# Optimization experiments

Measured on AMD Instinct MI355X. Metric: run time of the kernel, lower is better.

## Reference

```python
import jax, jax.numpy as jnp
import numpy as np

N_COMPANIES = 2000
HIDDEN = 256
HEADS = 8
LAYERS = 3
IN_DIM = 64
NEG_SLOPE = 0.2  # PyG GATConv default leaky_relu slope


def setup_inputs() -> dict:
    key = jax.random.key(0)
    ks = jax.random.split(key, 32)
    B, E = 64, 64000
    C = HIDDEN // HEADS
    emb_dim = HIDDEN // 4
    def lin(k, fo, fi):
        k1, k2 = jax.random.split(k)
        s = 1.0 / np.sqrt(fi)
        return (jax.random.uniform(k1, (fo, fi), jnp.float32, -s, s),
                jax.random.uniform(k2, (fo,), jnp.float32, -s, s))
    inp = {}
    inp['x'] = jax.random.normal(ks[0], (B, IN_DIM), jnp.float32)
    inp['company_indices'] = jax.random.randint(ks[1], (B,), 0, N_COMPANIES)
    inp['edge_index'] = jax.random.randint(ks[2], (2, E), 0, N_COMPANIES)
    inp['edge_attr'] = jax.random.uniform(ks[3], (E,), jnp.float32)
    inp['W_in'], inp['b_in'] = lin(ks[4], HIDDEN, IN_DIM)
    # stacked GAT params (all layers same shape)
    g = 0.05
    inp['gat_W'] = g * jax.random.normal(ks[5], (LAYERS, HEADS * C, HIDDEN), jnp.float32)
    inp['gat_att_src'] = g * jax.random.normal(ks[6], (LAYERS, HEADS, C), jnp.float32)
    inp['gat_att_dst'] = g * jax.random.normal(ks[7], (LAYERS, HEADS, C), jnp.float32)
    inp['gat_We'] = g * jax.random.normal(ks[8], (LAYERS, HEADS * C, 1), jnp.float32)
    inp['gat_att_edge'] = g * jax.random.normal(ks[9], (LAYERS, HEADS, C), jnp.float32)
    inp['gat_b'] = jnp.zeros((LAYERS, HEADS * C), jnp.float32)
    inp['emb'] = jax.random.normal(ks[10], (N_COMPANIES, emb_dim), jnp.float32)
    inp['W_fuse'], inp['b_fuse'] = lin(ks[11], HIDDEN, HIDDEN + emb_dim)
    inp['W_p1'], inp['b_p1'] = lin(ks[12], HIDDEN // 2, HIDDEN)
    inp['W_p2'], inp['b_p2'] = lin(ks[13], HIDDEN // 4, HIDDEN // 2)
    inp['W_p3'], inp['b_p3'] = lin(ks[14], 1, HIDDEN // 4)
    inp['W_d1'], inp['b_d1'] = lin(ks[15], HIDDEN // 2, HIDDEN)
    inp['W_d2'], inp['b_d2'] = lin(ks[16], HIDDEN // 4, HIDDEN // 2)
    inp['W_d3'], inp['b_d3'] = lin(ks[17], 1, HIDDEN // 4)
    return inp


def _gat_layer(xg, src, dst, ea, W, att_s, att_d, We, att_e, b, N):
    # xg: [N, F] node features; src/dst: [E2] (with self-loops); ea: [E2]
    H, C = att_s.shape
    xp = (xg @ W.T).reshape(N, H, C)
    a_s = jnp.sum(xp * att_s, -1)                       # [N, H]
    a_d = jnp.sum(xp * att_d, -1)                       # [N, H]
    ef = (ea[:, None] @ We.T).reshape(-1, H, C)         # [E2, H, C]
    a_e = jnp.sum(ef * att_e, -1)                       # [E2, H]
    logits = jax.nn.leaky_relu(a_s[src] + a_d[dst] + a_e, NEG_SLOPE)
    m = jax.ops.segment_max(logits, dst, num_segments=N)
    ex = jnp.exp(logits - m[dst])
    denom = jax.ops.segment_sum(ex, dst, num_segments=N)
    alpha = ex / (denom[dst] + 1e-16)                   # per-dst softmax
    out = jax.ops.segment_sum(alpha[:, :, None] * xp[src], dst, num_segments=N)
    return out.reshape(N, H * C) + b


def reference(x, company_indices, edge_index, edge_attr, W_in, b_in,
              gat_W, gat_att_src, gat_att_dst, gat_We, gat_att_edge, gat_b,
              emb, W_fuse, b_fuse, W_p1, b_p1, W_p2, b_p2, W_p3, b_p3,
              W_d1, b_d1, W_d2, b_d2, W_d3, b_d3):
    # eval mode: dropout is identity
    B = x.shape[0]
    N = emb.shape[0]
    h = jax.nn.relu(x @ W_in.T + b_in)                  # [B, hidden]
    # add self loops (PyG default, fill_value='mean' for edge_attr)
    loops = jnp.arange(N, dtype=edge_index.dtype)
    src = jnp.concatenate([edge_index[0], loops])
    dst = jnp.concatenate([edge_index[1], loops])
    ea = jnp.concatenate([edge_attr, jnp.full((N,), edge_attr.mean(), edge_attr.dtype)])

    def per_item(hi):
        g = jnp.broadcast_to(hi, (N, hi.shape[0]))
        for l in range(gat_W.shape[0]):
            g = jax.nn.relu(_gat_layer(g, src, dst, ea, gat_W[l], gat_att_src[l],
                                       gat_att_dst[l], gat_We[l], gat_att_edge[l], gat_b[l], N))
        return g

    gouts = jax.vmap(per_item)(h)                       # [B, N, hidden]
    comp_out = gouts[jnp.arange(B), company_indices]    # [B, hidden]
    comp_emb = emb[company_indices]                     # [B, hidden//4]
    fused = jax.nn.relu(jnp.concatenate([comp_out, comp_emb], -1) @ W_fuse.T + b_fuse)
    p = jax.nn.relu(fused @ W_p1.T + b_p1)
    p = jax.nn.relu(p @ W_p2.T + b_p2)
    price = (p @ W_p3.T + b_p3).squeeze(-1)
    d = jax.nn.relu(fused @ W_d1.T + b_d1)
    d = jax.nn.relu(d @ W_d2.T + b_d2)
    direction = jax.nn.sigmoid((d @ W_d3.T + b_d3)).squeeze(-1)
    return price, direction
```

## Files before the change

### kernel.cpp

```cpp
#include <hip/hip_runtime.h>
#include <math.h>


#define B_ITEMS 64

typedef _Float16 half_t;
typedef _Float16 half8 __attribute__((ext_vector_type(8)));

#define BIN   0
#define BGAT  256
#define BFUSE 1024
#define BP1   1280
#define BD1   1408
#define BP2   1536
#define BD2   1600
#define NBIAS 1664

template <int K, int G>
struct WFrag { half8 w[K / (8 * G)]; };

template <int K, int G>
__device__ __forceinline__ void load_frag(WFrag<K, G>& f,
                                          const float* __restrict__ W, int t) {
    const int c = t & (G - 1);
    const int o = t / G;
    const float4* __restrict__ W4 =
        reinterpret_cast<const float4*>(W + (size_t)o * K);
#pragma unroll
    for (int j = 0; j < K / (8 * G); ++j) {
        const int idx = j * G + c;
        float4 a = W4[2 * idx];
        float4 b = W4[2 * idx + 1];
        f.w[j] = half8{ (_Float16)a.x, (_Float16)a.y, (_Float16)a.z, (_Float16)a.w,
                        (_Float16)b.x, (_Float16)b.y, (_Float16)b.z, (_Float16)b.w };
    }
}

template <int M, int K, int G>
__device__ __forceinline__ void compute_frag(const WFrag<K, G>& f,
                                             const float* __restrict__ bias,
                                             const float* __restrict__ in,
                                             float* __restrict__ out,
                                             int t) {
    const int c = t & (G - 1);
    const int o = t / G;
    const float4* __restrict__ A4 = reinterpret_cast<const float4*>(in);
    float acc = 0.f;
#pragma unroll
    for (int j = 0; j < K / (8 * G); ++j) {
        const int idx = j * G + c;
        float4 a0 = A4[2 * idx];
        float4 a1 = A4[2 * idx + 1];
        half8 w = f.w[j];
        acc = fmaf((float)w[0], a0.x, acc);
        acc = fmaf((float)w[1], a0.y, acc);
        acc = fmaf((float)w[2], a0.z, acc);
        acc = fmaf((float)w[3], a0.w, acc);
        acc = fmaf((float)w[4], a1.x, acc);
        acc = fmaf((float)w[5], a1.y, acc);
        acc = fmaf((float)w[6], a1.z, acc);
        acc = fmaf((float)w[7], a1.w, acc);
    }
#pragma unroll
    for (int s = 1; s < G; s <<= 1) acc += __shfl_xor(acc, s, 64);
    if (c == 0) out[o] = fmaxf(acc + bias[o], 0.f);
}

extern "C" __global__ __launch_bounds__(1024, 4) void fin_gat_v8(
    const float* __restrict__ x,
    const int* __restrict__ cidx,
    const float* __restrict__ W_in,
    const float* __restrict__ b_in,
    const float* __restrict__ gat_W,
    const float* __restrict__ gat_b,
    const float* __restrict__ emb,
    const float* __restrict__ W_fuse,
    const float* __restrict__ b_fuse,
    const float* __restrict__ W_p1,
    const float* __restrict__ b_p1,
    const float* __restrict__ W_p2,
    const float* __restrict__ b_p2,
    const float* __restrict__ W_p3, const float* __restrict__ b_p3,
    const float* __restrict__ W_d1,
    const float* __restrict__ b_d1,
    const float* __restrict__ W_d2,
    const float* __restrict__ b_d2,
    const float* __restrict__ W_d3, const float* __restrict__ b_d3,
    float* __restrict__ out)
{
    __shared__ float bufA[320];
    __shared__ float bufB[320];
    __shared__ float bias_lds[NBIAS];

    const int b = blockIdx.x;
    const int t = threadIdx.x;

    WFrag<64, 4> f_in;
    load_frag(f_in, W_in, t);

    if (t < 64) {
        const int ci = cidx[b];
        bufA[t] = x[b * 64 + t];
        bufA[256 + t] = emb[(size_t)ci * 64 + t];
    }
    float wdot = 0.f, bdot = 0.f;
    if (t < 64)            wdot = W_p3[t];
    else if (t < 128)      wdot = W_d3[t - 64];
    if (t == 0)            bdot = b_p3[0];
    else if (t == 64)      bdot = b_d3[0];

#pragma unroll
    for (int i = t; i < NBIAS; i += 1024) {
        float v;
        if      (i < 256)  v = b_in[i];
        else if (i < 1024) v = gat_b[i - 256];
        else if (i < 1280) v = b_fuse[i - 1024];
        else if (i < 1408) v = b_p1[i - 1280];
        else if (i < 1536) v = b_d1[i - 1408];
        else if (i < 1600) v = b_p2[i - 1536];
        else               v = b_d2[i - 1600];
        bias_lds[i] = v;
    }
    __syncthreads();

    WFrag<256, 4> fg0;
    load_frag(fg0, gat_W + 0 * 65536, t);
    compute_frag<256, 64, 4>(f_in, bias_lds + BIN, bufA, bufB, t);
    __syncthreads();

    WFrag<256, 4> fg1;
    load_frag(fg1, gat_W + 1 * 65536, t);
    compute_frag<256, 256, 4>(fg0, bias_lds + BGAT, bufB, bufA, t);
    __syncthreads();

    WFrag<256, 4> fg2;
    load_frag(fg2, gat_W + 2 * 65536, t);
    compute_frag<256, 256, 4>(fg1, bias_lds + BGAT + 256, bufA, bufB, t);
    __syncthreads();

    WFrag<320, 4> f_fu;
    load_frag(f_fu, W_fuse, t);
    compute_frag<256, 256, 4>(fg2, bias_lds + BGAT + 512, bufB, bufA, t);
    __syncthreads();

    WFrag<256, 4> f_h1;
    load_frag(f_h1, (t < 512) ? W_p1 : W_d1, t & 511);
    compute_frag<256, 320, 4>(f_fu, bias_lds + BFUSE, bufA, bufB, t);
    __syncthreads();

    WFrag<128, 8> f_h2;
    load_frag(f_h2, (t < 512) ? W_p2 : W_d2, t & 511);
    if (t < 512) compute_frag<128, 256, 4>(f_h1, bias_lds + BP1, bufB, bufA, t);
    else         compute_frag<128, 256, 4>(f_h1, bias_lds + BD1, bufB, bufA + 192, t - 512);
    __syncthreads();

    if (t < 512) compute_frag<64, 128, 8>(f_h2, bias_lds + BP2, bufA, bufB, t);
    else         compute_frag<64, 128, 8>(f_h2, bias_lds + BD2, bufA + 192, bufB + 64, t - 512);
    __syncthreads();

    if (t < 64) {
        float v = wdot * bufB[t];
#pragma unroll
        for (int off = 32; off > 0; off >>= 1) v += __shfl_down(v, off, 64);
        if (t == 0) out[b] = v + bdot;
    } else if (t < 128) {
        const int u = t - 64;
        float v = wdot * bufB[64 + u];
#pragma unroll
        for (int off = 32; off > 0; off >>= 1) v += __shfl_down(v, off, 64);
        if (u == 0) {
            float z = v + bdot;
            out[B_ITEMS + b] = 1.0f / (1.0f + expf(-z));
        }
    }
}

extern "C" void kernel_launch(void* const* d_in, const int* in_sizes, int n_in,
                              void* d_out, int out_size, void* d_ws, size_t ws_size,
                              hipStream_t stream) {
    const float* x      = (const float*)d_in[0];
    const int*   cidx   = (const int*)  d_in[1];
    const float* W_in   = (const float*)d_in[4];
    const float* b_in   = (const float*)d_in[5];
    const float* gat_W  = (const float*)d_in[6];
    const float* gat_b  = (const float*)d_in[11];
    const float* emb    = (const float*)d_in[12];
    const float* W_fuse = (const float*)d_in[13];
    const float* b_fuse = (const float*)d_in[14];
    const float* W_p1   = (const float*)d_in[15];
    const float* b_p1   = (const float*)d_in[16];
    const float* W_p2   = (const float*)d_in[17];
    const float* b_p2   = (const float*)d_in[18];
    const float* W_p3   = (const float*)d_in[19];
    const float* b_p3   = (const float*)d_in[20];
    const float* W_d1   = (const float*)d_in[21];
    const float* b_d1   = (const float*)d_in[22];
    const float* W_d2   = (const float*)d_in[23];
    const float* b_d2   = (const float*)d_in[24];
    const float* W_d3   = (const float*)d_in[25];
    const float* b_d3   = (const float*)d_in[26];

    (void)d_ws; (void)ws_size;

    fin_gat_v8<<<B_ITEMS, 1024, 0, stream>>>(
        x, cidx, W_in, b_in, gat_W, gat_b, emb, W_fuse, b_fuse,
        W_p1, b_p1, W_p2, b_p2, W_p3, b_p3,
        W_d1, b_d1, W_d2, b_d2, W_d3, b_d3,
        (float*)d_out);
}
```

Before: 134.7 us.

## Stream weights through double-buffered LDS via async global-to-LDS loads

Replaces the per-thread fp16 register weight fragments with a double-buffered LDS pipeline. Each step issues global_load_lds copies of the next 64-row weight tile while the current tile is consumed from LDS in fp32, with explicit vmcnt waits and barriers between steps. The fuse layer is split into an accumulation pass plus a final pass over the embedding columns. This aims to overlap weight fetch with compute and drop the fp16 conversion, at the cost of many more barriers per block and 128KB of LDS per block, which limits residency to one block per CU.

```diff
diff --git a/kernel.cpp b/kernel.cpp
--- a/kernel.cpp
+++ b/kernel.cpp
@@ -3,9 +3,6 @@
 
 
 #define B_ITEMS 64
-
-typedef _Float16 half_t;
-typedef _Float16 half8 __attribute__((ext_vector_type(8)));
 
 #define BIN   0
 #define BGAT  256
@@ -16,57 +13,107 @@
 #define BD2   1600
 #define NBIAS 1664
 
-template <int K, int G>
-struct WFrag { half8 w[K / (8 * G)]; };
-
-template <int K, int G>
-__device__ __forceinline__ void load_frag(WFrag<K, G>& f,
-                                          const float* __restrict__ W, int t) {
+__device__ __forceinline__ void g2l16(const float* g, float* l) {
+    __builtin_amdgcn_global_load_lds(
+        (const __attribute__((address_space(1))) void*)g,
+        (__attribute__((address_space(3))) void*)l, 16, 0, 0);
+}
+
+template <int LOGQ>
+__device__ __forceinline__ void issue(const float* __restrict__ gbase, int rs,
+                                      float* lbuf, int t) {
+#pragma unroll
+    for (int i = 0; i < 4; ++i) {
+        const int n = i * 1024 + t;
+        const int r = n >> LOGQ;
+        const int q = n & ((1 << LOGQ) - 1);
+        g2l16(gbase + (size_t)r * rs + q * 4, lbuf + (size_t)n * 4);
+    }
+}
+
+__device__ __forceinline__ void issue_split(const float* __restrict__ gA,
+                                            const float* __restrict__ gB,
+                                            float* lbuf, int t) {
+#pragma unroll
+    for (int i = 0; i < 4; ++i) {
+        const int n = i * 1024 + t;
+        const int r = n >> 5;
+        const int q = n & 31;
+        const float* g = (r < 64) ? (gA + (size_t)r * 128 + q * 4)
+                                  : (gB + (size_t)(r - 64) * 128 + q * 4);
+        g2l16(g, lbuf + (size_t)n * 4);
+    }
+}
+
+template <int K, int G, int MODE>
+__device__ __forceinline__ void comp(const float* wt,
+                                     const float* vin,
+                                     float* vout,
+                                     const float* bias,
+                                     const float* accin,
+                                     int t) {
     const int c = t & (G - 1);
     const int o = t / G;
-    const float4* __restrict__ W4 =
-        reinterpret_cast<const float4*>(W + (size_t)o * K);
-#pragma unroll
-    for (int j = 0; j < K / (8 * G); ++j) {
+    const float4* W4 = reinterpret_cast<const float4*>(wt + (size_t)o * K);
+    const float4* A4 = reinterpret_cast<const float4*>(vin);
+    float acc = 0.f;
+#pragma unroll
+    for (int j = 0; j < K / (4 * G); ++j) {
         const int idx = j * G + c;
-        float4 a = W4[2 * idx];
-        float4 b = W4[2 * idx + 1];
-        f.w[j] = half8{ (_Float16)a.x, (_Float16)a.y, (_Float16)a.z, (_Float16)a.w,
-                        (_Float16)b.x, (_Float16)b.y, (_Float16)b.z, (_Float16)b.w };
-    }
-}
-
-template <int M, int K, int G>
-__device__ __forceinline__ void compute_frag(const WFrag<K, G>& f,
-                                             const float* __restrict__ bias,
-                                             const float* __restrict__ in,
-                                             float* __restrict__ out,
-                                             int t) {
-    const int c = t & (G - 1);
-    const int o = t / G;
-    const float4* __restrict__ A4 = reinterpret_cast<const float4*>(in);
+        float4 w = W4[idx];
+        float4 a = A4[idx];
+        acc = fmaf(w.x, a.x, acc);
+        acc = fmaf(w.y, a.y, acc);
+        acc = fmaf(w.z, a.z, acc);
+        acc = fmaf(w.w, a.w, acc);
+    }
+#pragma unroll
+    for (int s = 1; s < G; s <<= 1) acc += __shfl_xor(acc, s, 64);
+    if (c == 0) {
+        if constexpr (MODE == 0)      vout[o] = fmaxf(acc + bias[o], 0.f);
+        else if constexpr (MODE == 1) vout[o] = acc;
+        else                          vout[o] = fmaxf(acc + accin[o] + bias[o], 0.f);
+    }
+}
+
+__device__ __forceinline__ void comp_pd2(const float* wt, const float* vin,
+                                         float* vout, const float* bias_base,
+                                         int t) {
+    const int c = t & 7;
+    const int o = t >> 3;
+    const float* vi = vin + ((o < 64) ? 0 : 128);
+    const float* bi = (o < 64) ? (bias_base + BP2) : (bias_base + BD2 - 64);
+    const float4* W4 = reinterpret_cast<const float4*>(wt + (size_t)o * 128);
+    const float4* A4 = reinterpret_cast<const float4*>(vi);
     float acc = 0.f;
 #pragma unroll
-    for (int j = 0; j < K / (8 * G); ++j) {
-        const int idx = j * G + c;
-        float4 a0 = A4[2 * idx];
-        float4 a1 = A4[2 * idx + 1];
-        half8 w = f.w[j];
-        acc = fmaf((float)w[0], a0.x, acc);
-        acc = fmaf((float)w[1], a0.y, acc);
-        acc = fmaf((float)w[2], a0.z, acc);
-        acc = fmaf((float)w[3], a0.w, acc);
-        acc = fmaf((float)w[4], a1.x, acc);
-        acc = fmaf((float)w[5], a1.y, acc);
-        acc = fmaf((float)w[6], a1.z, acc);
-        acc = fmaf((float)w[7], a1.w, acc);
-    }
-#pragma unroll
-    for (int s = 1; s < G; s <<= 1) acc += __shfl_xor(acc, s, 64);
-    if (c == 0) out[o] = fmaxf(acc + bias[o], 0.f);
-}
-
-extern "C" __global__ __launch_bounds__(1024, 4) void fin_gat_v8(
+    for (int j = 0; j < 4; ++j) {
+        const int idx = j * 8 + c;
+        float4 w = W4[idx];
+        float4 a = A4[idx];
+        acc = fmaf(w.x, a.x, acc);
+        acc = fmaf(w.y, a.y, acc);
+        acc = fmaf(w.z, a.z, acc);
+        acc = fmaf(w.w, a.w, acc);
+    }
+#pragma unroll
+    for (int s = 1; s < 8; s <<= 1) acc += __shfl_xor(acc, s, 64);
+    if (c == 0) vout[o] = fmaxf(acc + bi[o], 0.f);
+}
+
+#define STEP(ISSUE_STMT, WAITN, COMP_STMT)                                   \
+    do {                                                                     \
+        ISSUE_STMT;                                                          \
+        asm volatile("s_waitcnt vmcnt(" WAITN ")" ::: "memory");             \
+        __builtin_amdgcn_sched_barrier(0);                                   \
+        __builtin_amdgcn_s_barrier();                                        \
+        COMP_STMT;                                                           \
+        asm volatile("s_waitcnt lgkmcnt(0)" ::: "memory");                   \
+        __builtin_amdgcn_s_barrier();                                        \
+        __builtin_amdgcn_sched_barrier(0);                                   \
+    } while (0)
+
+extern "C" __global__ __launch_bounds__(1024) void fin_gat_v10(
     const float* __restrict__ x,
     const int* __restrict__ cidx,
     const float* __restrict__ W_in,
@@ -88,20 +135,26 @@
     const float* __restrict__ W_d3, const float* __restrict__ b_d3,
     float* __restrict__ out)
 {
-    __shared__ float bufA[320];
-    __shared__ float bufB[320];
+    __shared__ float wbuf[2][16384];
+    __shared__ float vec0[256];
+    __shared__ float vec1[256];
+    __shared__ float xvec[64];
+    __shared__ float embvec[64];
+    __shared__ float accbuf[256];
     __shared__ float bias_lds[NBIAS];
 
     const int b = blockIdx.x;
     const int t = threadIdx.x;
-
-    WFrag<64, 4> f_in;
-    load_frag(f_in, W_in, t);
+    float* const wA = &wbuf[0][0];
+    float* const wB = &wbuf[1][0];
+    const float* const BL = bias_lds;
+
+    issue<4>(W_in, 64, wA, t);
 
     if (t < 64) {
         const int ci = cidx[b];
-        bufA[t] = x[b * 64 + t];
-        bufA[256 + t] = emb[(size_t)ci * 64 + t];
+        xvec[t]   = x[b * 64 + t];
+        embvec[t] = emb[(size_t)ci * 64 + t];
     }
     float wdot = 0.f, bdot = 0.f;
     if (t < 64)            wdot = W_p3[t];
@@ -123,49 +176,42 @@
     }
     __syncthreads();
 
-    WFrag<256, 4> fg0;
-    load_frag(fg0, gat_W + 0 * 65536, t);
-    compute_frag<256, 64, 4>(f_in, bias_lds + BIN, bufA, bufB, t);
-    __syncthreads();
-
-    WFrag<256, 4> fg1;
-    load_frag(fg1, gat_W + 1 * 65536, t);
-    compute_frag<256, 256, 4>(fg0, bias_lds + BGAT, bufB, bufA, t);
-    __syncthreads();
-
-    WFrag<256, 4> fg2;
-    load_frag(fg2, gat_W + 2 * 65536, t);
-    compute_frag<256, 256, 4>(fg1, bias_lds + BGAT + 256, bufA, bufB, t);
-    __syncthreads();
-
-    WFrag<320, 4> f_fu;
-    load_frag(f_fu, W_fuse, t);
-    compute_frag<256, 256, 4>(fg2, bias_lds + BGAT + 512, bufB, bufA, t);
-    __syncthreads();
-
-    WFrag<256, 4> f_h1;
-    load_frag(f_h1, (t < 512) ? W_p1 : W_d1, t & 511);
-    compute_frag<256, 320, 4>(f_fu, bias_lds + BFUSE, bufA, bufB, t);
-    __syncthreads();
-
-    WFrag<128, 8> f_h2;
-    load_frag(f_h2, (t < 512) ? W_p2 : W_d2, t & 511);
-    if (t < 512) compute_frag<128, 256, 4>(f_h1, bias_lds + BP1, bufB, bufA, t);
-    else         compute_frag<128, 256, 4>(f_h1, bias_lds + BD1, bufB, bufA + 192, t - 512);
-    __syncthreads();
-
-    if (t < 512) compute_frag<64, 128, 8>(f_h2, bias_lds + BP2, bufA, bufB, t);
-    else         compute_frag<64, 128, 8>(f_h2, bias_lds + BD2, bufA + 192, bufB + 64, t - 512);
-    __syncthreads();
+    const float* gW0 = gat_W;
+    const float* gW1 = gat_W + 65536;
+    const float* gW2 = gat_W + 131072;
+
+    STEP(issue<6>(gW0,            256, wB, t), "4", (comp<64, 4, 0>(wA, xvec, vec0, BL + BIN, nullptr, t)));
+    STEP(issue<6>(gW0 +  64*256,  256, wA, t), "4", (comp<256,16, 0>(wB, vec0, vec1 +   0, BL + BGAT +   0, nullptr, t)));
+    STEP(issue<6>(gW0 + 128*256,  256, wB, t), "4", (comp<256,16, 0>(wA, vec0, vec1 +  64, BL + BGAT +  64, nullptr, t)));
+    STEP(issue<6>(gW0 + 192*256,  256, wA, t), "4", (comp<256,16, 0>(wB, vec0, vec1 + 128, BL + BGAT + 128, nullptr, t)));
+    STEP(issue<6>(gW1,            256, wB, t), "4", (comp<256,16, 0>(wA, vec0, vec1 + 192, BL + BGAT + 192, nullptr, t)));
+    STEP(issue<6>(gW1 +  64*256,  256, wA, t), "4", (comp<256,16, 0>(wB, vec1, vec0 +   0, BL + BGAT + 256,       nullptr, t)));
+    STEP(issue<6>(gW1 + 128*256,  256, wB, t), "4", (comp<256,16, 0>(wA, vec1, vec0 +  64, BL + BGAT + 256 +  64, nullptr, t)));
+    STEP(issue<6>(gW1 + 192*256,  256, wA, t), "4", (comp<256,16, 0>(wB, vec1, vec0 + 128, BL + BGAT + 256 + 128, nullptr, t)));
+    STEP(issue<6>(gW2,            256, wB, t), "4", (comp<256,16, 0>(wA, vec1, vec0 + 192, BL + BGAT + 256 + 192, nullptr, t)));
+    STEP(issue<6>(gW2 +  64*256,  256, wA, t), "4", (comp<256,16, 0>(wB, vec0, vec1 +   0, BL + BGAT + 512,       nullptr, t)));
+    STEP(issue<6>(gW2 + 128*256,  256, wB, t), "4", (comp<256,16, 0>(wA, vec0, vec1 +  64, BL + BGAT + 512 +  64, nullptr, t)));
+    STEP(issue<6>(gW2 + 192*256,  256, wA, t), "4", (comp<256,16, 0>(wB, vec0, vec1 + 128, BL + BGAT + 512 + 128, nullptr, t)));
+    STEP(issue<6>(W_fuse,         320, wB, t), "4", (comp<256,16, 0>(wA, vec0, vec1 + 192, BL + BGAT + 512 + 192, nullptr, t)));
+    STEP(issue<6>(W_fuse +  64*320, 320, wA, t), "4", (comp<256,16, 1>(wB, vec1, accbuf +   0, nullptr, nullptr, t)));
+    STEP(issue<6>(W_fuse + 128*320, 320, wB, t), "4", (comp<256,16, 1>(wA, vec1, accbuf +  64, nullptr, nullptr, t)));
+    STEP(issue<6>(W_fuse + 192*320, 320, wA, t), "4", (comp<256,16, 1>(wB, vec1, accbuf + 128, nullptr, nullptr, t)));
+    STEP(issue<4>(W_fuse + 256,     320, wB, t), "4", (comp<256,16, 1>(wA, vec1, accbuf + 192, nullptr, nullptr, t)));
+    STEP(issue<6>(W_p1,           256, wA, t), "4", (comp<64, 4, 2>(wB, embvec, vec0, BL + BFUSE, accbuf, t)));
+    STEP(issue<6>(W_p1 + 64*256,  256, wB, t), "4", (comp<256,16, 0>(wA, vec0, vec1 +   0, BL + BP1,      nullptr, t)));
+    STEP(issue<6>(W_d1,           256, wA, t), "4", (comp<256,16, 0>(wB, vec0, vec1 +  64, BL + BP1 + 64, nullptr, t)));
+    STEP(issue<6>(W_d1 + 64*256,  256, wB, t), "4", (comp<256,16, 0>(wA, vec0, vec1 + 128, BL + BD1,      nullptr, t)));
+    STEP(issue_split(W_p2, W_d2,       wA, t), "4", (comp<256,16, 0>(wB, vec0, vec1 + 192, BL + BD1 + 64, nullptr, t)));
+    STEP((void)0,                              "0", (comp_pd2(wA, vec1, vec0, BL, t)));
 
     if (t < 64) {
-        float v = wdot * bufB[t];
+        float v = wdot * vec0[t];
 #pragma unroll
         for (int off = 32; off > 0; off >>= 1) v += __shfl_down(v, off, 64);
         if (t == 0) out[b] = v + bdot;
     } else if (t < 128) {
         const int u = t - 64;
-        float v = wdot * bufB[64 + u];
+        float v = wdot * vec0[64 + u];
 #pragma unroll
         for (int off = 32; off > 0; off >>= 1) v += __shfl_down(v, off, 64);
         if (u == 0) {
@@ -202,7 +248,7 @@
 
     (void)d_ws; (void)ws_size;
 
-    fin_gat_v8<<<B_ITEMS, 1024, 0, stream>>>(
+    fin_gat_v10<<<B_ITEMS, 1024, 0, stream>>>(
         x, cidx, W_in, b_in, gat_W, gat_b, emb, W_fuse, b_fuse,
         W_p1, b_p1, W_p2, b_p2, W_p3, b_p3,
         W_d1, b_d1, W_d2, b_d2, W_d3, b_d3,
```

Result: faster. 131.9 us (-2.1%).

## Stream fp32 weights per layer instead of prefetching fp16 register fragments

Applied to the files above, without the earlier changes.

Removes the register-resident fp16 weight fragments that were prefetched one layer ahead, and instead streams fp32 weight rows directly from global memory inside each layer in chunks of four float4 loads, with a non-unrolled outer loop. Biases are read directly per output rather than staged in LDS, and the interleaved c-stride layout changes to per-float4 striding. This lowers register pressure and drops fp16 conversion, but loses the cross-layer prefetch overlap, so each layer's weight-load latency is exposed between barriers.

```diff
diff --git a/kernel.cpp b/kernel.cpp
--- a/kernel.cpp
+++ b/kernel.cpp
@@ -4,69 +4,44 @@
 
 #define B_ITEMS 64
 
-typedef _Float16 half_t;
-typedef _Float16 half8 __attribute__((ext_vector_type(8)));
-
-#define BIN   0
-#define BGAT  256
-#define BFUSE 1024
-#define BP1   1280
-#define BD1   1408
-#define BP2   1536
-#define BD2   1600
-#define NBIAS 1664
-
-template <int K, int G>
-struct WFrag { half8 w[K / (8 * G)]; };
-
-template <int K, int G>
-__device__ __forceinline__ void load_frag(WFrag<K, G>& f,
-                                          const float* __restrict__ W, int t) {
-    const int c = t & (G - 1);
-    const int o = t / G;
-    const float4* __restrict__ W4 =
-        reinterpret_cast<const float4*>(W + (size_t)o * K);
+template <int K, int G, bool RELU>
+__device__ __forceinline__ void layer_g(
+    const float* __restrict__ Wrow,
+    float bv,
+    const float* __restrict__ vin,
+    float* __restrict__ vout,
+    int o, int c) {
+    const float4* __restrict__ W4 = reinterpret_cast<const float4*>(Wrow);
+    const float4* __restrict__ A4 = reinterpret_cast<const float4*>(vin);
+    constexpr int NJ = K / (4 * G);
+    constexpr int CH = (NJ >= 4) ? 4 : NJ;
+    float acc = 0.f;
+#pragma unroll 1
+    for (int jj = 0; jj < NJ; jj += CH) {
+        float4 w[CH], a[CH];
 #pragma unroll
-    for (int j = 0; j < K / (8 * G); ++j) {
-        const int idx = j * G + c;
-        float4 a = W4[2 * idx];
-        float4 b = W4[2 * idx + 1];
-        f.w[j] = half8{ (_Float16)a.x, (_Float16)a.y, (_Float16)a.z, (_Float16)a.w,
-                        (_Float16)b.x, (_Float16)b.y, (_Float16)b.z, (_Float16)b.w };
+        for (int u = 0; u < CH; ++u) {
+            const int idx = (jj + u) * G + c;
+            w[u] = W4[idx];
+            a[u] = A4[idx];
+        }
+#pragma unroll
+        for (int u = 0; u < CH; ++u) {
+            acc = fmaf(w[u].x, a[u].x, acc);
+            acc = fmaf(w[u].y, a[u].y, acc);
+            acc = fmaf(w[u].z, a[u].z, acc);
+            acc = fmaf(w[u].w, a[u].w, acc);
+        }
+    }
+#pragma unroll
+    for (int s = 1; s < G; s <<= 1) acc += __shfl_xor(acc, s, 64);
+    if (c == 0) {
+        const float r = acc + bv;
+        vout[o] = RELU ? fmaxf(r, 0.f) : r;
     }
 }
 
-template <int M, int K, int G>
-__device__ __forceinline__ void compute_frag(const WFrag<K, G>& f,
-                                             const float* __restrict__ bias,
-                                             const float* __restrict__ in,
-                                             float* __restrict__ out,
-                                             int t) {
-    const int c = t & (G - 1);
-    const int o = t / G;
-    const float4* __restrict__ A4 = reinterpret_cast<const float4*>(in);
-    float acc = 0.f;
-#pragma unroll
-    for (int j = 0; j < K / (8 * G); ++j) {
-        const int idx = j * G + c;
-        float4 a0 = A4[2 * idx];
-        float4 a1 = A4[2 * idx + 1];
-        half8 w = f.w[j];
-        acc = fmaf((float)w[0], a0.x, acc);
-        acc = fmaf((float)w[1], a0.y, acc);
-        acc = fmaf((float)w[2], a0.z, acc);
-        acc = fmaf((float)w[3], a0.w, acc);
-        acc = fmaf((float)w[4], a1.x, acc);
-        acc = fmaf((float)w[5], a1.y, acc);
-        acc = fmaf((float)w[6], a1.z, acc);
-        acc = fmaf((float)w[7], a1.w, acc);
-    }
-#pragma unroll
-    for (int s = 1; s < G; s <<= 1) acc += __shfl_xor(acc, s, 64);
-    if (c == 0) out[o] = fmaxf(acc + bias[o], 0.f);
-}
-
-extern "C" __global__ __launch_bounds__(1024, 4) void fin_gat_v8(
+extern "C" __global__ __launch_bounds__(1024) void fin_gat_v11(
     const float* __restrict__ x,
     const int* __restrict__ cidx,
     const float* __restrict__ W_in,
@@ -88,84 +63,71 @@
     const float* __restrict__ W_d3, const float* __restrict__ b_d3,
     float* __restrict__ out)
 {
-    __shared__ float bufA[320];
-    __shared__ float bufB[320];
-    __shared__ float bias_lds[NBIAS];
+    __shared__ float vecA[320];
+    __shared__ float vecB[256];
+    __shared__ float xvec[64];
 
     const int b = blockIdx.x;
     const int t = threadIdx.x;
-
-    WFrag<64, 4> f_in;
-    load_frag(f_in, W_in, t);
+    const int o4 = t >> 2, c4 = t & 3;
 
     if (t < 64) {
         const int ci = cidx[b];
-        bufA[t] = x[b * 64 + t];
-        bufA[256 + t] = emb[(size_t)ci * 64 + t];
+        xvec[t] = x[b * 64 + t];
+        vecA[256 + t] = emb[(size_t)ci * 64 + t];
     }
     float wdot = 0.f, bdot = 0.f;
     if (t < 64)            wdot = W_p3[t];
     else if (t < 128)      wdot = W_d3[t - 64];
     if (t == 0)            bdot = b_p3[0];
     else if (t == 64)      bdot = b_d3[0];
+    __syncthreads();
 
-#pragma unroll
-    for (int i = t; i < NBIAS; i += 1024) {
-        float v;
-        if      (i < 256)  v = b_in[i];
-        else if (i < 1024) v = gat_b[i - 256];
-        else if (i < 1280) v = b_fuse[i - 1024];
-        else if (i < 1408) v = b_p1[i - 1280];
-        else if (i < 1536) v = b_d1[i - 1408];
-        else if (i < 1600) v = b_p2[i - 1536];
-        else               v = b_d2[i - 1600];
-        bias_lds[i] = v;
+    layer_g<64, 4, true>(W_in + (size_t)o4 * 64, b_in[o4], xvec, vecB, o4, c4);
+    __syncthreads();
+
+    layer_g<256, 4, true>(gat_W + (size_t)o4 * 256, gat_b[o4],
+                          vecB, vecA, o4, c4);
+    __syncthreads();
+
+    layer_g<256, 4, true>(gat_W + 65536 + (size_t)o4 * 256, gat_b[256 + o4],
+                          vecA, vecB, o4, c4);
+    __syncthreads();
+
+    layer_g<256, 4, true>(gat_W + 131072 + (size_t)o4 * 256, gat_b[512 + o4],
+                          vecB, vecA, o4, c4);
+    __syncthreads();
+
+    layer_g<320, 4, true>(W_fuse + (size_t)o4 * 320, b_fuse[o4],
+                          vecA, vecB, o4, c4);
+    __syncthreads();
+
+    {
+        const float* Wr = (o4 < 128) ? (W_p1 + (size_t)o4 * 256)
+                                     : (W_d1 + (size_t)(o4 - 128) * 256);
+        const float bv = (o4 < 128) ? b_p1[o4] : b_d1[o4 - 128];
+        layer_g<256, 4, true>(Wr, bv, vecB, vecA, o4, c4);
     }
     __syncthreads();
 
-    WFrag<256, 4> fg0;
-    load_frag(fg0, gat_W + 0 * 65536, t);
-    compute_frag<256, 64, 4>(f_in, bias_lds + BIN, bufA, bufB, t);
-    __syncthreads();
-
-    WFrag<256, 4> fg1;
-    load_frag(fg1, gat_W + 1 * 65536, t);
-    compute_frag<256, 256, 4>(fg0, bias_lds + BGAT, bufB, bufA, t);
-    __syncthreads();
-
-    WFrag<256, 4> fg2;
-    load_frag(fg2, gat_W + 2 * 65536, t);
-    compute_frag<256, 256, 4>(fg1, bias_lds + BGAT + 256, bufA, bufB, t);
-    __syncthreads();
-
-    WFrag<320, 4> f_fu;
-    load_frag(f_fu, W_fuse, t);
-    compute_frag<256, 256, 4>(fg2, bias_lds + BGAT + 512, bufB, bufA, t);
-    __syncthreads();
-
-    WFrag<256, 4> f_h1;
-    load_frag(f_h1, (t < 512) ? W_p1 : W_d1, t & 511);
-    compute_frag<256, 320, 4>(f_fu, bias_lds + BFUSE, bufA, bufB, t);
-    __syncthreads();
-
-    WFrag<128, 8> f_h2;
-    load_frag(f_h2, (t < 512) ? W_p2 : W_d2, t & 511);
-    if (t < 512) compute_frag<128, 256, 4>(f_h1, bias_lds + BP1, bufB, bufA, t);
-    else         compute_frag<128, 256, 4>(f_h1, bias_lds + BD1, bufB, bufA + 192, t - 512);
-    __syncthreads();
-
-    if (t < 512) compute_frag<64, 128, 8>(f_h2, bias_lds + BP2, bufA, bufB, t);
-    else         compute_frag<64, 128, 8>(f_h2, bias_lds + BD2, bufA + 192, bufB + 64, t - 512);
+    {
+        const int o8 = t >> 3, c8 = t & 7;
+        const float* Wr = (o8 < 64) ? (W_p2 + (size_t)o8 * 128)
+                                    : (W_d2 + (size_t)(o8 - 64) * 128);
+        const float bv = (o8 < 64) ? b_p2[o8] : b_d2[o8 - 64];
+        const float* vi = vecA + ((o8 < 64) ? 0 : 128);
+        layer_g<128, 8, true>(Wr, bv, vi, vecB, o8, c8);
+    }
     __syncthreads();
 
     if (t < 64) {
-        float v = wdot * bufB[t];
+        float v = wdot * vecB[t];
 #pragma unroll
         for (int off = 32; off > 0; off >>= 1) v += __shfl_down(v, off, 64);
         if (t == 0) out[b] = v + bdot;
     } else if (t < 128) {
         const int u = t - 64;
-        float v = wdot * bufB[64 + u];
+        float v = wdot * vecB[64 + u];
 #pragma unroll
         for (int off = 32; off > 0; off >>= 1) v += __shfl_down(v, off, 64);
         if (u == 0) {
@@ -202,7 +164,7 @@
 
     (void)d_ws; (void)ws_size;
 
-    fin_gat_v8<<<B_ITEMS, 1024, 0, stream>>>(
+    fin_gat_v11<<<B_ITEMS, 1024, 0, stream>>>(
         x, cidx, W_in, b_in, gat_W, gat_b, emb, W_fuse, b_fuse,
         W_p1, b_p1, W_p2, b_p2, W_p3, b_p3,
         W_d1, b_d1, W_d2, b_d2, W_d3, b_d3,
```

Result: faster. 124.8 us (-7.3%).
